# Kernel optimization log

Measured on AMD Instinct MI355X. Metric: run time of the kernel, lower is better.

The kernel has to match this reference:

```python
import jax, jax.numpy as jnp
import numpy as np

B, T, D, H = 2, 2048, 1024, 16
DK = D // H


def setup_inputs() -> dict:
    key = jax.random.key(0)
    ks = jax.random.split(key, 11)
    s = 0.02
    inp = {
        "q": jax.random.normal(ks[0], (B, T, D), jnp.float32),
        "k": jax.random.normal(ks[1], (B, T, D), jnp.float32),
        "v": jax.random.normal(ks[2], (B, T, D), jnp.float32),
        # True = masked (causal), broadcast over batch and heads
        "attn_mask": jnp.triu(jnp.ones((T, T), bool), k=1)[None, None],
        "Wq": jax.random.normal(ks[3], (D, D), jnp.float32) * s,
        "bq": jnp.zeros((D,), jnp.float32),
        "Wk": jax.random.normal(ks[4], (D, D), jnp.float32) * s,
        "bk": jnp.zeros((D,), jnp.float32),
        "Wv": jax.random.normal(ks[5], (D, D), jnp.float32) * s,
        "bv": jnp.zeros((D,), jnp.float32),
        "Wo": jax.random.normal(ks[6], (D, D), jnp.float32) * s,
        "bo": jnp.zeros((D,), jnp.float32),
    }
    return inp


def _split_heads(x):
    # [B,T,D] -> [B,H,T,DK]
    return x.reshape(B, T, H, DK).transpose(0, 2, 1, 3)


def reference(q, k, v, attn_mask, Wq, bq, Wk, bk, Wv, bv, Wo, bo):
    query = _split_heads(q @ Wq.T + bq)
    key_ = _split_heads(k @ Wk.T + bk)
    value = _split_heads(v @ Wv.T + bv)
    scale = 1.0 / jnp.sqrt(jnp.asarray(DK, query.dtype))
    scores = jnp.einsum("bhqd,bhkd->bhqk", query, key_) * scale
    scores = jnp.where(attn_mask, -jnp.inf, scores)
    probs = jax.nn.softmax(scores, axis=-1)  # dropout p=0.0 (eval)
    ctx = jnp.einsum("bhqk,bhkd->bhqd", probs, value)
    ctx = ctx.transpose(0, 2, 1, 3).reshape(B, T, D)
    return ctx @ Wo.T + bo
```

## Files before the change

kernel.cpp:

```cpp
#include <hip/hip_runtime.h>
#include <stdint.h>

#define Bsz 2
#define Tseq 2048
#define Dmodel 1024
#define Hn 16
#define DKd 64

typedef __bf16 bf16;
typedef bf16 bf16x8 __attribute__((ext_vector_type(8)));
typedef float f32x4 __attribute__((ext_vector_type(4)));

__device__ inline void gld_lds16(const void* g, void* l) {
  __builtin_amdgcn_global_load_lds(
      (const __attribute__((address_space(1))) uint32_t*)g,
      (__attribute__((address_space(3))) uint32_t*)l, 16, 0, 0);
}

__device__ inline void pack4_store(bf16* dst, float a, float b, float c, float d) {
  union { bf16 h[4]; uint2 u; } pk;
  pk.h[0] = (bf16)a; pk.h[1] = (bf16)b; pk.h[2] = (bf16)c; pk.h[3] = (bf16)d;
  *(uint2*)dst = pk.u;
}

struct CvtArgs {
  const float* src[7];
  bf16* dst[7];
  int n4[7];
};

__global__ void __launch_bounds__(256) cvt_f32_bf16(CvtArgs a) {
  const int z = blockIdx.y;
  const float4* s = (const float4*)a.src[z];
  uint2* d = (uint2*)a.dst[z];
  const int n4 = a.n4[z];
  for (int i = blockIdx.x * 256 + threadIdx.x; i < n4; i += gridDim.x * 256) {
    float4 v = s[i];
    union { bf16 h[4]; uint2 u; } pk;
    pk.h[0] = (bf16)v.x; pk.h[1] = (bf16)v.y;
    pk.h[2] = (bf16)v.z; pk.h[3] = (bf16)v.w;
    d[i] = pk.u;
  }
}

struct GemmArgs {
  const bf16* A[3];
  const bf16* W[3];
  const float* bias[3];
  void* out[3];
  int mode[3];
  float scale[3];
};

__global__ void __launch_bounds__(256) gemm_qkv(GemmArgs g) {
  const int l = blockIdx.x;
  const int z = l >> 8;
  const int r = l & 255;
  const int mt = (r & 7) * 4 + (r >> 6);
  const int nt = (r >> 3) & 7;
  const bf16* __restrict__ A = g.A[z];
  const bf16* __restrict__ W = g.W[z];
  const float* __restrict__ bias = g.bias[z];
  const int mode = g.mode[z];
  const float scl = g.scale[z];

  __shared__ __align__(16) bf16 As[128 * 32];
  __shared__ __align__(16) bf16 Bs[128 * 32];

  const int tid = threadIdx.x;
  const int w = tid >> 6, lane = tid & 63;
  const int l15 = lane & 15, quad = lane >> 4;
  const int wm = (w >> 1) * 64, wn = (w & 1) * 64;
  const int m0 = mt * 128, n0 = nt * 128;

  f32x4 zero = {0.f, 0.f, 0.f, 0.f};
  f32x4 acc[4][4];
#pragma unroll
  for (int mi = 0; mi < 4; ++mi)
#pragma unroll
    for (int ni = 0; ni < 4; ++ni) acc[mi][ni] = zero;

  for (int k0 = 0; k0 < Dmodel; k0 += 32) {
    __syncthreads();
#pragma unroll
    for (int p = 0; p < 2; ++p) {
      const int c = p * 256 + tid;
      const int row = c >> 2, ko = (c & 3) * 8;
      gld_lds16(A + (size_t)(m0 + row) * Dmodel + k0 + ko, (void*)(As + c * 8));
      gld_lds16(W + (size_t)(n0 + row) * Dmodel + k0 + ko, (void*)(Bs + c * 8));
    }
    __syncthreads();

    bf16x8 af[4], bfr[4];
#pragma unroll
    for (int i = 0; i < 4; ++i) {
      af[i]  = *(const bf16x8*)(As + (wm + i * 16 + l15) * 32 + quad * 8);
      bfr[i] = *(const bf16x8*)(Bs + (wn + i * 16 + l15) * 32 + quad * 8);
    }
#pragma unroll
    for (int mi = 0; mi < 4; ++mi)
#pragma unroll
      for (int ni = 0; ni < 4; ++ni)
        acc[mi][ni] = __builtin_amdgcn_mfma_f32_16x16x32_bf16(af[mi], bfr[ni],
                                                              acc[mi][ni], 0, 0, 0);
  }

#pragma unroll
  for (int mi = 0; mi < 4; ++mi) {
#pragma unroll
    for (int r2 = 0; r2 < 4; ++r2) {
      const int m = m0 + wm + mi * 16 + quad * 4 + r2;
      const int bb = m >> 11, tt = m & 2047;
#pragma unroll
      for (int ni = 0; ni < 4; ++ni) {
        const int n = n0 + wn + ni * 16 + l15;
        const float val = (acc[mi][ni][r2] + bias[n]) * scl;
        bf16* o = (bf16*)g.out[z];
        const int hh = n >> 6, dk = n & 63;
        if (mode == 0) {
          o[((size_t)(bb * Hn + hh) * Tseq + tt) * DKd + dk] = (bf16)val;
        } else {
          o[((size_t)(bb * Hn + hh) * DKd + dk) * Tseq + tt] = (bf16)val;
        }
      }
    }
  }
}

__global__ void __launch_bounds__(256) gemm_out64(const bf16* __restrict__ A,
                                                  const bf16* __restrict__ W,
                                                  const float* __restrict__ bias,
                                                  float* __restrict__ out) {
  const int l = blockIdx.x;
  const int mt = (l & 7) * 8 + (l >> 6);
  const int nt = (l >> 3) & 7;

  __shared__ __align__(16) bf16 As[64 * 32];
  __shared__ __align__(16) bf16 Bs[128 * 32];

  const int tid = threadIdx.x;
  const int w = tid >> 6, lane = tid & 63;
  const int l15 = lane & 15, quad = lane >> 4;
  const int wm = (w >> 1) * 32, wn = (w & 1) * 64;
  const int m0 = mt * 64, n0 = nt * 128;

  f32x4 zero = {0.f, 0.f, 0.f, 0.f};
  f32x4 acc[2][4];
#pragma unroll
  for (int mi = 0; mi < 2; ++mi)
#pragma unroll
    for (int ni = 0; ni < 4; ++ni) acc[mi][ni] = zero;

  for (int k0 = 0; k0 < Dmodel; k0 += 32) {
    __syncthreads();
    {
      const int c = tid;
      const int row = c >> 2, ko = (c & 3) * 8;
      gld_lds16(A + (size_t)(m0 + row) * Dmodel + k0 + ko, (void*)(As + c * 8));
    }
#pragma unroll
    for (int p = 0; p < 2; ++p) {
      const int c = p * 256 + tid;
      const int row = c >> 2, ko = (c & 3) * 8;
      gld_lds16(W + (size_t)(n0 + row) * Dmodel + k0 + ko, (void*)(Bs + c * 8));
    }
    __syncthreads();

    bf16x8 af[2], bfr[4];
#pragma unroll
    for (int i = 0; i < 2; ++i)
      af[i] = *(const bf16x8*)(As + (wm + i * 16 + l15) * 32 + quad * 8);
#pragma unroll
    for (int i = 0; i < 4; ++i)
      bfr[i] = *(const bf16x8*)(Bs + (wn + i * 16 + l15) * 32 + quad * 8);
#pragma unroll
    for (int mi = 0; mi < 2; ++mi)
#pragma unroll
      for (int ni = 0; ni < 4; ++ni)
        acc[mi][ni] = __builtin_amdgcn_mfma_f32_16x16x32_bf16(af[mi], bfr[ni],
                                                              acc[mi][ni], 0, 0, 0);
  }

#pragma unroll
  for (int mi = 0; mi < 2; ++mi)
#pragma unroll
    for (int r = 0; r < 4; ++r) {
      const int m = m0 + wm + mi * 16 + quad * 4 + r;
#pragma unroll
      for (int ni = 0; ni < 4; ++ni) {
        const int n = n0 + wn + ni * 16 + l15;
        out[(size_t)m * Dmodel + n] = acc[mi][ni][r] + bias[n];
      }
    }
}

__global__ void __launch_bounds__(256) attn_fused(const bf16* __restrict__ Q,
                                                  const bf16* __restrict__ K,
                                                  const bf16* __restrict__ Vt,
                                                  bf16* __restrict__ ctx) {
  __shared__ __align__(16) bf16 Ks[8 * 128 * 8];
  __shared__ __align__(16) bf16 Vs[16 * 64 * 8];
  __shared__ __align__(16) bf16 plds[4][16][136];

  const int tid = threadIdx.x;
  const int w = tid >> 6, lane = tid & 63;
  const int l15 = lane & 15, quad = lane >> 4;

  const int l = blockIdx.x;
  const int qt = (Tseq / 64 - 1) - (l >> 5);
  const int hb = l & 31;
  const int h = hb & 15, b = hb >> 4;
  const int bh = b * Hn + h;
  const int qb = qt * 64 + w * 16;

  const bf16* Qb = Q + (size_t)bh * Tseq * DKd;
  const bf16* Kb = K + (size_t)bh * Tseq * DKd;
  const bf16* Vb = Vt + (size_t)bh * DKd * Tseq;

  bf16x8 aq0 = *(const bf16x8*)(Qb + (size_t)(qb + l15) * DKd + quad * 8);
  bf16x8 aq1 = *(const bf16x8*)(Qb + (size_t)(qb + l15) * DKd + 32 + quad * 8);

  f32x4 zero = {0.f, 0.f, 0.f, 0.f};
  f32x4 oacc[4];
#pragma unroll
  for (int nd = 0; nd < 4; ++nd) oacc[nd] = zero;
  f32x4 lacc = zero;

  bf16x8 onesf;
#pragma unroll
  for (int i = 0; i < 8; ++i) onesf[i] = (bf16)1.0f;

  const int qmax = qt * 64 + 48;
  for (int j0 = 0; j0 <= qmax; j0 += 128) {
    __syncthreads();
#pragma unroll
    for (int p = 0; p < 4; ++p) {
      const int c = p * 256 + tid;
      gld_lds16(Kb + (size_t)(j0 + (c & 127)) * DKd + (c >> 7) * 8,
                (void*)(Ks + c * 8));
      gld_lds16(Vb + (size_t)(c & 63) * Tseq + j0 + (c >> 6) * 8,
                (void*)(Vs + c * 8));
    }
    __syncthreads();

    if (j0 + 128 <= qb) {
      f32x4 s[8];
#pragma unroll
      for (int ct = 0; ct < 8; ++ct) s[ct] = zero;
#pragma unroll
      for (int ct = 0; ct < 8; ++ct) {
        bf16x8 bk0 = *(const bf16x8*)(Ks + ((quad)*128 + ct * 16 + l15) * 8);
        bf16x8 bk1 = *(const bf16x8*)(Ks + ((4 + quad) * 128 + ct * 16 + l15) * 8);
        s[ct] = __builtin_amdgcn_mfma_f32_16x16x32_bf16(bk0, aq0, s[ct], 0, 0, 0);
        s[ct] = __builtin_amdgcn_mfma_f32_16x16x32_bf16(bk1, aq1, s[ct], 0, 0, 0);
      }
#pragma unroll
      for (int ct = 0; ct < 8; ++ct)
        pack4_store(&plds[w][l15][ct * 16 + quad * 4],
                    exp2f(s[ct][0]), exp2f(s[ct][1]),
                    exp2f(s[ct][2]), exp2f(s[ct][3]));
#pragma unroll
      for (int kc = 0; kc < 4; ++kc) {
        bf16x8 bp = *(const bf16x8*)(&plds[w][l15][kc * 32 + quad * 8]);
        lacc = __builtin_amdgcn_mfma_f32_16x16x32_bf16(onesf, bp, lacc, 0, 0, 0);
#pragma unroll
        for (int nd = 0; nd < 4; ++nd) {
          bf16x8 bv = *(const bf16x8*)(Vs + ((kc * 4 + quad) * 64 + nd * 16 + l15) * 8);
          oacc[nd] = __builtin_amdgcn_mfma_f32_16x16x32_bf16(bv, bp, oacc[nd], 0, 0, 0);
        }
      }
    } else if (j0 <= qb) {
      const int ctl = ((qb - j0) >> 4) + 1;
      const int kclim = (ctl + 1) >> 1;
      for (int ct = 0; ct < ctl; ++ct) {
        bf16x8 bk0 = *(const bf16x8*)(Ks + ((quad)*128 + ct * 16 + l15) * 8);
        bf16x8 bk1 = *(const bf16x8*)(Ks + ((4 + quad) * 128 + ct * 16 + l15) * 8);
        f32x4 s = zero;
        s = __builtin_amdgcn_mfma_f32_16x16x32_bf16(bk0, aq0, s, 0, 0, 0);
        s = __builtin_amdgcn_mfma_f32_16x16x32_bf16(bk1, aq1, s, 0, 0, 0);
        float p[4];
#pragma unroll
        for (int r = 0; r < 4; ++r) {
          p[r] = exp2f(s[r]);
          if (ct == ctl - 1 && (j0 + ct * 16 + quad * 4 + r > qb + l15)) p[r] = 0.f;
        }
        pack4_store(&plds[w][l15][ct * 16 + quad * 4], p[0], p[1], p[2], p[3]);
      }
      if (ctl < 8)
        pack4_store(&plds[w][l15][ctl * 16 + quad * 4], 0.f, 0.f, 0.f, 0.f);
      for (int kc = 0; kc < kclim; ++kc) {
        bf16x8 bp = *(const bf16x8*)(&plds[w][l15][kc * 32 + quad * 8]);
        lacc = __builtin_amdgcn_mfma_f32_16x16x32_bf16(onesf, bp, lacc, 0, 0, 0);
#pragma unroll
        for (int nd = 0; nd < 4; ++nd) {
          bf16x8 bv = *(const bf16x8*)(Vs + ((kc * 4 + quad) * 64 + nd * 16 + l15) * 8);
          oacc[nd] = __builtin_amdgcn_mfma_f32_16x16x32_bf16(bv, bp, oacc[nd], 0, 0, 0);
        }
      }
    }
  }

  const float inv = 1.0f / lacc[0];
  bf16* cb = ctx + (size_t)(b * Tseq + qb + l15) * Dmodel + h * DKd + quad * 4;
#pragma unroll
  for (int nd = 0; nd < 4; ++nd)
    pack4_store(cb + nd * 16, oacc[nd][0] * inv, oacc[nd][1] * inv,
                oacc[nd][2] * inv, oacc[nd][3] * inv);
}

extern "C" void kernel_launch(void* const* d_in, const int* in_sizes, int n_in,
                              void* d_out, int out_size, void* d_ws, size_t ws_size,
                              hipStream_t stream) {
  const float* q = (const float*)d_in[0];
  const float* k = (const float*)d_in[1];
  const float* v = (const float*)d_in[2];
  const float* Wq = (const float*)d_in[4];
  const float* bq = (const float*)d_in[5];
  const float* Wk = (const float*)d_in[6];
  const float* bk = (const float*)d_in[7];
  const float* Wv = (const float*)d_in[8];
  const float* bv = (const float*)d_in[9];
  const float* Wo = (const float*)d_in[10];
  const float* bo = (const float*)d_in[11];

  char* ws = (char*)d_ws;
  const size_t MB = 1024 * 1024;
  bf16* Wq_b = (bf16*)(ws + 0 * MB);
  bf16* Wk_b = (bf16*)(ws + 2 * MB);
  bf16* Wv_b = (bf16*)(ws + 4 * MB);
  bf16* Wo_b = (bf16*)(ws + 6 * MB);
  bf16* q_b  = (bf16*)(ws + 8 * MB);
  bf16* k_b  = (bf16*)(ws + 16 * MB);
  bf16* v_b  = (bf16*)(ws + 24 * MB);
  bf16* Qh   = (bf16*)(ws + 32 * MB);
  bf16* Kh   = (bf16*)(ws + 40 * MB);
  bf16* Vt   = (bf16*)(ws + 48 * MB);
  bf16* ctx  = (bf16*)(ws + 8 * MB);

  const int NACT4 = (Bsz * Tseq * Dmodel) / 4;
  const int NW4 = (Dmodel * Dmodel) / 4;

  CvtArgs ca;
  ca.src[0] = q;  ca.dst[0] = q_b;  ca.n4[0] = NACT4;
  ca.src[1] = k;  ca.dst[1] = k_b;  ca.n4[1] = NACT4;
  ca.src[2] = v;  ca.dst[2] = v_b;  ca.n4[2] = NACT4;
  ca.src[3] = Wq; ca.dst[3] = Wq_b; ca.n4[3] = NW4;
  ca.src[4] = Wk; ca.dst[4] = Wk_b; ca.n4[4] = NW4;
  ca.src[5] = Wv; ca.dst[5] = Wv_b; ca.n4[5] = NW4;
  ca.src[6] = Wo; ca.dst[6] = Wo_b; ca.n4[6] = NW4;
  cvt_f32_bf16<<<dim3(512, 7), 256, 0, stream>>>(ca);

  const float SC = 0.125f * 1.4426950408889634f;
  GemmArgs ga;
  ga.A[0] = q_b; ga.W[0] = Wq_b; ga.bias[0] = bq; ga.out[0] = Qh; ga.mode[0] = 0; ga.scale[0] = SC;
  ga.A[1] = k_b; ga.W[1] = Wk_b; ga.bias[1] = bk; ga.out[1] = Kh; ga.mode[1] = 0; ga.scale[1] = 1.f;
  ga.A[2] = v_b; ga.W[2] = Wv_b; ga.bias[2] = bv; ga.out[2] = Vt; ga.mode[2] = 1; ga.scale[2] = 1.f;
  gemm_qkv<<<dim3(768), 256, 0, stream>>>(ga);

  attn_fused<<<dim3((Tseq / 64) * Hn * Bsz), 256, 0, stream>>>(Qh, Kh, Vt, ctx);

  gemm_out64<<<dim3(512), 256, 0, stream>>>(ctx, Wo_b, bo, (float*)d_out);
}
```

Measured before the change: 231.2 us.

## Replace QKV and output GEMMs with 256x256 double-buffered pipelined GEMM kernel

Replaces the 128x128 QKV GEMM and the 64x128 output GEMM with one 256x256-tile, 512-thread kernel. It uses a 64-wide K step, XOR-swizzled LDS, and double-buffered global-to-LDS loads interleaved with MFMA phases under explicit barriers and setprio. The output projection reuses the same kernel through a new fp32 row-major store mode. Larger tiles cut global traffic per FLOP and the pipelining hides load latency. The cost is fewer workgroups: 192 for QKV and only 64 for the output projection, which may underfill the GPU.

```diff
diff --git a/kernel.cpp b/kernel.cpp
--- a/kernel.cpp
+++ b/kernel.cpp
@@ -52,146 +52,189 @@
   float scale[3];
 };
 
-__global__ void __launch_bounds__(256) gemm_qkv(GemmArgs g) {
-  const int l = blockIdx.x;
-  const int z = l >> 8;
-  const int r = l & 255;
-  const int mt = (r & 7) * 4 + (r >> 6);
-  const int nt = (r >> 3) & 7;
+#define PHASE_MID()                                          \
+  do {                                                       \
+    __builtin_amdgcn_s_barrier();                            \
+    asm volatile("s_waitcnt lgkmcnt(0)" ::: "memory");       \
+    __builtin_amdgcn_sched_barrier(0);                       \
+  } while (0)
+#define PHASE_END() __builtin_amdgcn_s_barrier()
+
+template <int MH>
+__device__ __forceinline__ void readA(bf16x8 (&aR)[4][2], const bf16* tile,
+                                      int wm, int l15, int quad) {
+#pragma unroll
+  for (int f = 0; f < 4; ++f)
+#pragma unroll
+    for (int ks = 0; ks < 2; ++ks) {
+      const int row = wm + MH * 64 + f * 16 + l15;
+      const int c = ks * 4 + quad;
+      aR[f][ks] = *(const bf16x8*)(tile + row * 64 + ((c ^ (row & 7)) << 3));
+    }
+}
+
+template <int NH>
+__device__ __forceinline__ void readB(bf16x8 (&bR)[2][2], const bf16* tile,
+                                      int wn, int l15, int quad) {
+#pragma unroll
+  for (int nf = 0; nf < 2; ++nf)
+#pragma unroll
+    for (int ks = 0; ks < 2; ++ks) {
+      const int row = wn + NH * 32 + nf * 16 + l15;
+      const int c = ks * 4 + quad;
+      bR[nf][ks] = *(const bf16x8*)(tile + row * 64 + ((c ^ (row & 7)) << 3));
+    }
+}
+
+template <int MH, int NH>
+__device__ __forceinline__ void qmfma(f32x4 (&acc)[8][4],
+                                      const bf16x8 (&aR)[4][2],
+                                      const bf16x8 (&bR)[2][2]) {
+  __builtin_amdgcn_s_setprio(1);
+#pragma unroll
+  for (int f = 0; f < 4; ++f)
+#pragma unroll
+    for (int nf = 0; nf < 2; ++nf)
+#pragma unroll
+      for (int ks = 0; ks < 2; ++ks)
+        acc[MH * 4 + f][NH * 2 + nf] = __builtin_amdgcn_mfma_f32_16x16x32_bf16(
+            aR[f][ks], bR[nf][ks], acc[MH * 4 + f][NH * 2 + nf], 0, 0, 0);
+  __builtin_amdgcn_s_setprio(0);
+}
+
+__device__ __forceinline__ void stageHalf(const bf16* __restrict__ g, int grow0,
+                                          int gcol0, bf16* lds, int tid) {
+#pragma unroll
+  for (int rr = 0; rr < 2; ++rr) {
+    const int row = rr * 64 + (tid >> 3);
+    const int c = (tid & 7) ^ (row & 7);
+    gld_lds16(g + (size_t)(grow0 + row) * Dmodel + gcol0 + c * 8,
+              (void*)(lds + rr * 4096 + tid * 8));
+  }
+}
+
+__global__ void __launch_bounds__(512, 2) gemm256(GemmArgs g) {
+  const int bid = blockIdx.x;
+  const int cpx = (int)gridDim.x >> 3;
+  const int wg = (bid & 7) * cpx + (bid >> 3);
+  const int z = wg >> 6;
+  const int r = wg & 63;
+  const int mt = r >> 2, nt = r & 3;
+
   const bf16* __restrict__ A = g.A[z];
   const bf16* __restrict__ W = g.W[z];
   const float* __restrict__ bias = g.bias[z];
   const int mode = g.mode[z];
   const float scl = g.scale[z];
-
-  __shared__ __align__(16) bf16 As[128 * 32];
-  __shared__ __align__(16) bf16 Bs[128 * 32];
+  const int m0 = mt * 256, n0 = nt * 256;
+
+  __shared__ __align__(16) bf16 As_[2][256 * 64];
+  __shared__ __align__(16) bf16 Bs_[2][256 * 64];
 
   const int tid = threadIdx.x;
   const int w = tid >> 6, lane = tid & 63;
   const int l15 = lane & 15, quad = lane >> 4;
-  const int wm = (w >> 1) * 64, wn = (w & 1) * 64;
-  const int m0 = mt * 128, n0 = nt * 128;
+  const int wm = (w >> 2) * 128, wn = (w & 3) * 64;
 
   f32x4 zero = {0.f, 0.f, 0.f, 0.f};
-  f32x4 acc[4][4];
-#pragma unroll
-  for (int mi = 0; mi < 4; ++mi)
-#pragma unroll
-    for (int ni = 0; ni < 4; ++ni) acc[mi][ni] = zero;
-
-  for (int k0 = 0; k0 < Dmodel; k0 += 32) {
-    __syncthreads();
-#pragma unroll
-    for (int p = 0; p < 2; ++p) {
-      const int c = p * 256 + tid;
-      const int row = c >> 2, ko = (c & 3) * 8;
-      gld_lds16(A + (size_t)(m0 + row) * Dmodel + k0 + ko, (void*)(As + c * 8));
-      gld_lds16(W + (size_t)(n0 + row) * Dmodel + k0 + ko, (void*)(Bs + c * 8));
-    }
-    __syncthreads();
-
-    bf16x8 af[4], bfr[4];
-#pragma unroll
-    for (int i = 0; i < 4; ++i) {
-      af[i]  = *(const bf16x8*)(As + (wm + i * 16 + l15) * 32 + quad * 8);
-      bfr[i] = *(const bf16x8*)(Bs + (wn + i * 16 + l15) * 32 + quad * 8);
-    }
-#pragma unroll
-    for (int mi = 0; mi < 4; ++mi)
-#pragma unroll
-      for (int ni = 0; ni < 4; ++ni)
-        acc[mi][ni] = __builtin_amdgcn_mfma_f32_16x16x32_bf16(af[mi], bfr[ni],
-                                                              acc[mi][ni], 0, 0, 0);
-  }
-
-#pragma unroll
-  for (int mi = 0; mi < 4; ++mi) {
-#pragma unroll
-    for (int r2 = 0; r2 < 4; ++r2) {
-      const int m = m0 + wm + mi * 16 + quad * 4 + r2;
+  f32x4 acc[8][4];
+#pragma unroll
+  for (int mf = 0; mf < 8; ++mf)
+#pragma unroll
+    for (int nf = 0; nf < 4; ++nf) acc[mf][nf] = zero;
+
+  bf16x8 aR[4][2], bR0[2][2], bR1[2][2];
+
+  stageHalf(W, n0 + 0,   0,  Bs_[0], tid);
+  stageHalf(W, n0 + 128, 0,  Bs_[0] + 128 * 64, tid);
+  stageHalf(A, m0 + 0,   0,  As_[0], tid);
+  stageHalf(A, m0 + 128, 0,  As_[0] + 128 * 64, tid);
+  stageHalf(W, n0 + 0,   64, Bs_[1], tid);
+  stageHalf(W, n0 + 128, 64, Bs_[1] + 128 * 64, tid);
+  asm volatile("s_waitcnt vmcnt(4)" ::: "memory");
+  __builtin_amdgcn_s_barrier();
+
+  for (int i = 0; i < 7; ++i) {
+    const int kA = (2 * i + 1) * 64;
+    const int kB = (2 * i + 2) * 64;
+    const int kC = (2 * i + 3) * 64;
+    readA<0>(aR, As_[0], wm, l15, quad);
+    readB<0>(bR0, Bs_[0], wn, l15, quad);
+    stageHalf(A, m0 + 0, kA, As_[1], tid);
+    PHASE_MID(); qmfma<0, 0>(acc, aR, bR0); PHASE_END();
+    readB<1>(bR1, Bs_[0], wn, l15, quad);
+    stageHalf(A, m0 + 128, kA, As_[1] + 128 * 64, tid);
+    PHASE_MID(); qmfma<0, 1>(acc, aR, bR1); PHASE_END();
+    readA<1>(aR, As_[0], wm, l15, quad);
+    stageHalf(W, n0 + 0, kB, Bs_[0], tid);
+    PHASE_MID(); qmfma<1, 1>(acc, aR, bR1); PHASE_END();
+    stageHalf(W, n0 + 128, kB, Bs_[0] + 128 * 64, tid);
+    PHASE_MID(); qmfma<1, 0>(acc, aR, bR0);
+    asm volatile("s_waitcnt vmcnt(4)" ::: "memory");
+    PHASE_END();
+    readA<0>(aR, As_[1], wm, l15, quad);
+    readB<0>(bR0, Bs_[1], wn, l15, quad);
+    stageHalf(A, m0 + 0, kB, As_[0], tid);
+    PHASE_MID(); qmfma<0, 0>(acc, aR, bR0); PHASE_END();
+    readB<1>(bR1, Bs_[1], wn, l15, quad);
+    stageHalf(A, m0 + 128, kB, As_[0] + 128 * 64, tid);
+    PHASE_MID(); qmfma<0, 1>(acc, aR, bR1); PHASE_END();
+    readA<1>(aR, As_[1], wm, l15, quad);
+    stageHalf(W, n0 + 0, kC, Bs_[1], tid);
+    PHASE_MID(); qmfma<1, 1>(acc, aR, bR1); PHASE_END();
+    stageHalf(W, n0 + 128, kC, Bs_[1] + 128 * 64, tid);
+    PHASE_MID(); qmfma<1, 0>(acc, aR, bR0);
+    asm volatile("s_waitcnt vmcnt(4)" ::: "memory");
+    PHASE_END();
+  }
+
+  {
+    const int kA = 15 * 64;
+    readA<0>(aR, As_[0], wm, l15, quad);
+    readB<0>(bR0, Bs_[0], wn, l15, quad);
+    stageHalf(A, m0 + 0, kA, As_[1], tid);
+    PHASE_MID(); qmfma<0, 0>(acc, aR, bR0); PHASE_END();
+    readB<1>(bR1, Bs_[0], wn, l15, quad);
+    stageHalf(A, m0 + 128, kA, As_[1] + 128 * 64, tid);
+    PHASE_MID(); qmfma<0, 1>(acc, aR, bR1); PHASE_END();
+    readA<1>(aR, As_[0], wm, l15, quad);
+    PHASE_MID(); qmfma<1, 1>(acc, aR, bR1); PHASE_END();
+    PHASE_MID(); qmfma<1, 0>(acc, aR, bR0);
+    asm volatile("s_waitcnt vmcnt(0)" ::: "memory");
+    PHASE_END();
+    readA<0>(aR, As_[1], wm, l15, quad);
+    readB<0>(bR0, Bs_[1], wn, l15, quad);
+    PHASE_MID(); qmfma<0, 0>(acc, aR, bR0); PHASE_END();
+    readB<1>(bR1, Bs_[1], wn, l15, quad);
+    PHASE_MID(); qmfma<0, 1>(acc, aR, bR1); PHASE_END();
+    readA<1>(aR, As_[1], wm, l15, quad);
+    PHASE_MID(); qmfma<1, 1>(acc, aR, bR1); PHASE_END();
+    PHASE_MID(); qmfma<1, 0>(acc, aR, bR0);
+  }
+
+#pragma unroll
+  for (int mf = 0; mf < 8; ++mf) {
+#pragma unroll
+    for (int rr = 0; rr < 4; ++rr) {
+      const int m = m0 + wm + mf * 16 + quad * 4 + rr;
       const int bb = m >> 11, tt = m & 2047;
 #pragma unroll
-      for (int ni = 0; ni < 4; ++ni) {
-        const int n = n0 + wn + ni * 16 + l15;
-        const float val = (acc[mi][ni][r2] + bias[n]) * scl;
-        bf16* o = (bf16*)g.out[z];
-        const int hh = n >> 6, dk = n & 63;
-        if (mode == 0) {
-          o[((size_t)(bb * Hn + hh) * Tseq + tt) * DKd + dk] = (bf16)val;
+      for (int nf = 0; nf < 4; ++nf) {
+        const int n = n0 + wn + nf * 16 + l15;
+        const float val = (acc[mf][nf][rr] + bias[n]) * scl;
+        if (mode == 2) {
+          ((float*)g.out[z])[(size_t)m * Dmodel + n] = val;
         } else {
-          o[((size_t)(bb * Hn + hh) * DKd + dk) * Tseq + tt] = (bf16)val;
+          bf16* o = (bf16*)g.out[z];
+          const int hh = n >> 6, dk = n & 63;
+          if (mode == 0)
+            o[((size_t)(bb * Hn + hh) * Tseq + tt) * DKd + dk] = (bf16)val;
+          else
+            o[((size_t)(bb * Hn + hh) * DKd + dk) * Tseq + tt] = (bf16)val;
         }
       }
     }
   }
-}
-
-__global__ void __launch_bounds__(256) gemm_out64(const bf16* __restrict__ A,
-                                                  const bf16* __restrict__ W,
-                                                  const float* __restrict__ bias,
-                                                  float* __restrict__ out) {
-  const int l = blockIdx.x;
-  const int mt = (l & 7) * 8 + (l >> 6);
-  const int nt = (l >> 3) & 7;
-
-  __shared__ __align__(16) bf16 As[64 * 32];
-  __shared__ __align__(16) bf16 Bs[128 * 32];
-
-  const int tid = threadIdx.x;
-  const int w = tid >> 6, lane = tid & 63;
-  const int l15 = lane & 15, quad = lane >> 4;
-  const int wm = (w >> 1) * 32, wn = (w & 1) * 64;
-  const int m0 = mt * 64, n0 = nt * 128;
-
-  f32x4 zero = {0.f, 0.f, 0.f, 0.f};
-  f32x4 acc[2][4];
-#pragma unroll
-  for (int mi = 0; mi < 2; ++mi)
-#pragma unroll
-    for (int ni = 0; ni < 4; ++ni) acc[mi][ni] = zero;
-
-  for (int k0 = 0; k0 < Dmodel; k0 += 32) {
-    __syncthreads();
-    {
-      const int c = tid;
-      const int row = c >> 2, ko = (c & 3) * 8;
-      gld_lds16(A + (size_t)(m0 + row) * Dmodel + k0 + ko, (void*)(As + c * 8));
-    }
-#pragma unroll
-    for (int p = 0; p < 2; ++p) {
-      const int c = p * 256 + tid;
-      const int row = c >> 2, ko = (c & 3) * 8;
-      gld_lds16(W + (size_t)(n0 + row) * Dmodel + k0 + ko, (void*)(Bs + c * 8));
-    }
-    __syncthreads();
-
-    bf16x8 af[2], bfr[4];
-#pragma unroll
-    for (int i = 0; i < 2; ++i)
-      af[i] = *(const bf16x8*)(As + (wm + i * 16 + l15) * 32 + quad * 8);
-#pragma unroll
-    for (int i = 0; i < 4; ++i)
-      bfr[i] = *(const bf16x8*)(Bs + (wn + i * 16 + l15) * 32 + quad * 8);
-#pragma unroll
-    for (int mi = 0; mi < 2; ++mi)
-#pragma unroll
-      for (int ni = 0; ni < 4; ++ni)
-        acc[mi][ni] = __builtin_amdgcn_mfma_f32_16x16x32_bf16(af[mi], bfr[ni],
-                                                              acc[mi][ni], 0, 0, 0);
-  }
-
-#pragma unroll
-  for (int mi = 0; mi < 2; ++mi)
-#pragma unroll
-    for (int r = 0; r < 4; ++r) {
-      const int m = m0 + wm + mi * 16 + quad * 4 + r;
-#pragma unroll
-      for (int ni = 0; ni < 4; ++ni) {
-        const int n = n0 + wn + ni * 16 + l15;
-        out[(size_t)m * Dmodel + n] = acc[mi][ni][r] + bias[n];
-      }
-    }
 }
 
 __global__ void __launch_bounds__(256) attn_fused(const bf16* __restrict__ Q,
@@ -355,9 +398,13 @@
   ga.A[0] = q_b; ga.W[0] = Wq_b; ga.bias[0] = bq; ga.out[0] = Qh; ga.mode[0] = 0; ga.scale[0] = SC;
   ga.A[1] = k_b; ga.W[1] = Wk_b; ga.bias[1] = bk; ga.out[1] = Kh; ga.mode[1] = 0; ga.scale[1] = 1.f;
   ga.A[2] = v_b; ga.W[2] = Wv_b; ga.bias[2] = bv; ga.out[2] = Vt; ga.mode[2] = 1; ga.scale[2] = 1.f;
-  gemm_qkv<<<dim3(768), 256, 0, stream>>>(ga);
+  gemm256<<<dim3(192), 512, 0, stream>>>(ga);
 
   attn_fused<<<dim3((Tseq / 64) * Hn * Bsz), 256, 0, stream>>>(Qh, Kh, Vt, ctx);
 
-  gemm_out64<<<dim3(512), 256, 0, stream>>>(ctx, Wo_b, bo, (float*)d_out);
-}
+  GemmArgs go;
+  go.A[0] = ctx;  go.W[0] = Wo_b; go.bias[0] = bo; go.out[0] = d_out; go.mode[0] = 2; go.scale[0] = 1.f;
+  go.A[1] = ctx;  go.W[1] = Wo_b; go.bias[1] = bo; go.out[1] = d_out; go.mode[1] = 2; go.scale[1] = 1.f;
+  go.A[2] = ctx;  go.W[2] = Wo_b; go.bias[2] = bo; go.out[2] = d_out; go.mode[2] = 2; go.scale[2] = 1.f;
+  gemm256<<<dim3(64), 512, 0, stream>>>(go);
+}
```

Result: slower. 280.5 us (+21.3%).
